# Kernel optimization log

Hardware: AMD Instinct MI355X
Metric: run time of the kernel (lower is better)

Reference implementation:

```python
import jax, jax.numpy as jnp
import numpy as np

B, S, D = 4, 4096, 1024
DC = 1024  # d_chunk (defaults to d_model)
NUM_CLASSES = 4


def setup_inputs() -> dict:
    key = jax.random.key(0)
    ks = jax.random.split(key, 8)
    init = lambda k, shape: (jax.random.normal(k, shape, jnp.float32) * 0.02)
    return {
        "h": jax.random.normal(ks[0], (B, S, D), jnp.float32),
        "pseudo_labels": jax.random.randint(ks[1], (B, S), 0, NUM_CLASSES, jnp.int32),
        "Wl": init(ks[2], (D, NUM_CLASSES)), "bl": jnp.zeros((NUM_CLASSES,), jnp.float32),
        "Wq": init(ks[3], (D, DC)), "bq": jnp.zeros((DC,), jnp.float32),
        "Wk": init(ks[4], (D, DC)), "bk": jnp.zeros((DC,), jnp.float32),
        "Wv": init(ks[5], (D, D)), "bv": jnp.zeros((D,), jnp.float32),
        "Wo": init(ks[6], (D, D)), "bo": jnp.zeros((D,), jnp.float32),
    }


def _chunk_starts(labels):
    """BIOS chunking: label 0=B starts a chunk extended by following 1=I's;
    labels 1 (orphan I), 2=O, 3=S are singleton chunks. Returns bool [B,S]
    marking chunk starts. Parallel replacement for the torch while-loop."""
    def step(ext, lab):  # ext[b]: previous token can be extended by an I
        cont = (lab == 1) & ext          # this token continues prev chunk
        new_ext = (lab == 0) | cont      # B, or a continuing I, is extendable
        return new_ext, ~cont            # non-continuing token starts a chunk
    init = jnp.zeros(labels.shape[0], dtype=bool)
    _, starts_t = jax.lax.scan(step, init, labels.T)  # scan over seq axis
    return starts_t.T  # [B, S]


def reference(h, pseudo_labels, Wl, bl, Wq, bq, Wk, bk, Wv, bv, Wo, bo):
    b, s, d = h.shape
    dc = Wq.shape[1]

    logits = h @ Wl + bl                                  # [B,S,4]
    logp = jax.nn.log_softmax(logits, axis=-1)
    loss = -jnp.mean(jnp.take_along_axis(logp, pseudo_labels[..., None], axis=-1))

    pred = jnp.argmax(logits, axis=-1).astype(jnp.int32)  # [B,S]
    starts = _chunk_starts(pred)
    seg = jnp.cumsum(starts.astype(jnp.int32), axis=1) - 1  # segment id per token

    # Segment-mean pooling, padded to S possible chunks per batch element.
    seg_sum = jax.vmap(lambda x, ids: jax.ops.segment_sum(x, ids, num_segments=s))(h, seg)
    counts = jax.vmap(lambda ids: jax.ops.segment_sum(jnp.ones((s,), h.dtype), ids, num_segments=s))(seg)
    chunk_emb = seg_sum / jnp.maximum(counts, 1.0)[..., None]  # [B,S,D]
    valid = counts > 0                                         # [B,S]

    q = h @ Wq + bq              # [B,S,DC]
    k = chunk_emb @ Wk + bk      # [B,C,DC]
    v = chunk_emb @ Wv + bv      # [B,C,D]
    scale = jnp.asarray(1.0 / np.sqrt(dc), h.dtype)
    scores = jnp.einsum('bsd,bcd->bsc', q, k) * scale
    scores = jnp.where(valid[:, None, :], scores, jnp.asarray(-1e30, h.dtype))
    attn = jax.nn.softmax(scores, axis=-1)
    attended = jnp.einsum('bsc,bcd->bsd', attn, v)
    ch_out = attended @ Wo + bo
    return ch_out, loss
```

## Files before the change

kernel.cpp:

```cpp
#include <hip/hip_runtime.h>

typedef unsigned short u16;
typedef __attribute__((ext_vector_type(8))) short short8;
typedef __attribute__((ext_vector_type(8))) unsigned short ushort8;
typedef __attribute__((ext_vector_type(4))) unsigned short ushort4v;
typedef __attribute__((ext_vector_type(4))) float f32x4;

#define NB 4
#define SS 4096
#define DD 1024
#define CFENCE asm volatile("" ::: "memory")

__device__ __forceinline__ u16 f2bf(float x) {
  unsigned u = __builtin_bit_cast(unsigned, x);
  u = (u + 0x7FFFu + ((u >> 16) & 1u)) >> 16;
  return (u16)u;
}
__device__ __forceinline__ float bf2f(u16 b) {
  unsigned u = ((unsigned)b) << 16;
  return __builtin_bit_cast(float, u);
}
__device__ __forceinline__ void gload16(const void* g, void* l) {
  __builtin_amdgcn_global_load_lds((const __attribute__((address_space(1))) void*)g,
                                   (__attribute__((address_space(3))) void*)l, 16, 0, 0);
}
__device__ __forceinline__ int xcd_swz(int bid, int nwg) {
  const int x = bid & 7, idx = bid >> 3;
  const int q = nwg >> 3, r = nwg & 7;
  return (x < r ? x * (q + 1) : r * (q + 1) + (x - r) * q) + idx;
}

__global__ __launch_bounds__(256) void k_logits(
    const float* __restrict__ h, const int* __restrict__ lab,
    const float* __restrict__ Wl, const float* __restrict__ bl,
    u16* __restrict__ h16, int* __restrict__ pred, float* __restrict__ lossPart)
{
  const int t = threadIdx.x, w = t >> 6, lane = t & 63;
  const int tok = blockIdx.x * 4 + w;
  const float4* h4p = (const float4*)(h + (size_t)tok * DD);
  const float4* wl4 = (const float4*)Wl;
  float p0 = 0.f, p1 = 0.f, p2 = 0.f, p3 = 0.f;
#pragma unroll
  for (int i = 0; i < 4; ++i) {
    const int d = i * 256 + lane * 4;
    float4 hv = h4p[i * 64 + lane];
    ushort4v hb;
    hb[0] = f2bf(hv.x); hb[1] = f2bf(hv.y); hb[2] = f2bf(hv.z); hb[3] = f2bf(hv.w);
    *(ushort4v*)(h16 + (size_t)tok * DD + d) = hb;
    float4 w0 = wl4[d], w1 = wl4[d + 1], w2 = wl4[d + 2], w3 = wl4[d + 3];
    p0 += hv.x * w0.x + hv.y * w1.x + hv.z * w2.x + hv.w * w3.x;
    p1 += hv.x * w0.y + hv.y * w1.y + hv.z * w2.y + hv.w * w3.y;
    p2 += hv.x * w0.z + hv.y * w1.z + hv.z * w2.z + hv.w * w3.z;
    p3 += hv.x * w0.w + hv.y * w1.w + hv.z * w2.w + hv.w * w3.w;
  }
#pragma unroll
  for (int m = 32; m; m >>= 1) {
    p0 += __shfl_xor(p0, m); p1 += __shfl_xor(p1, m);
    p2 += __shfl_xor(p2, m); p3 += __shfl_xor(p3, m);
  }
  __shared__ float ls[4];
  if (lane == 0) {
    float l[4] = {p0 + bl[0], p1 + bl[1], p2 + bl[2], p3 + bl[3]};
    int bi = 0; float bv = l[0];
#pragma unroll
    for (int c = 1; c < 4; ++c) if (l[c] > bv) { bv = l[c]; bi = c; }
    pred[tok] = bi;
    float se = 0.f;
#pragma unroll
    for (int c = 0; c < 4; ++c) se += expf(l[c] - bv);
    float lse = bv + logf(se);
    ls[w] = lse - l[lab[tok]];
  }
  __syncthreads();
  if (t == 0) lossPart[blockIdx.x] = ls[0] + ls[1] + ls[2] + ls[3];
}

__global__ __launch_bounds__(256) void k_wconv(
    const float* __restrict__ W0, const float* __restrict__ W1,
    const float* __restrict__ W2, const float* __restrict__ W3,
    u16* __restrict__ Wt)
{
  const int gid = blockIdx.x * 256 + threadIdx.x;
  const int mat = gid >> 20;
  const int rem = gid & ((1 << 20) - 1);
  const int n = rem >> 10, k = rem & 1023;
  const float* W = (mat == 0) ? W0 : (mat == 1) ? W1 : (mat == 2) ? W2 : W3;
  Wt[((size_t)mat << 20) + (size_t)n * 1024 + k] = f2bf(W[(size_t)k * 1024 + n]);
}

__global__ __launch_bounds__(256) void k_scan(
    const int* __restrict__ pred, int* __restrict__ cstart, int* __restrict__ ccnt)
{
  const int b = blockIdx.x, t = threadIdx.x;
  const int4* p4 = (const int4*)(pred + (size_t)b * SS);
  int labv[16];
#pragma unroll
  for (int i = 0; i < 4; ++i) {
    int4 v = p4[t * 4 + i];
    labv[i * 4 + 0] = v.x; labv[i * 4 + 1] = v.y;
    labv[i * 4 + 2] = v.z; labv[i * 4 + 3] = v.w;
  }
  int A = 0, Bc = 1;
#pragma unroll
  for (int e = 0; e < 16; ++e) {
    int a = (labv[e] == 0), bb = (labv[e] == 1);
    A = a | (bb & A);
    Bc = bb & Bc;
  }
  __shared__ int sA[256], sB[256], sC[256];
  sA[t] = A; sB[t] = Bc;
  __syncthreads();
  for (int off = 1; off < 256; off <<= 1) {
    int pa = 0, pb = 1;
    if (t >= off) { pa = sA[t - off]; pb = sB[t - off]; }
    __syncthreads();
    A = A | (Bc & pa); Bc = Bc & pb;
    sA[t] = A; sB[t] = Bc;
    __syncthreads();
  }
  const int extIn = (t == 0) ? 0 : sA[t - 1];
  int ext = extIn, nst = 0;
#pragma unroll
  for (int e = 0; e < 16; ++e) {
    int cont = (labv[e] == 1) & ext;
    nst += !cont;
    ext = (labv[e] == 0) | cont;
  }
  sC[t] = nst;
  __syncthreads();
  int tot = nst;
  for (int off = 1; off < 256; off <<= 1) {
    int pc = 0;
    if (t >= off) pc = sC[t - off];
    __syncthreads();
    tot += pc;
    sC[t] = tot;
    __syncthreads();
  }
  const int base = tot - nst;
  const int total = sC[255];
  if (t == 0) { ccnt[b] = total; cstart[b * (SS + 1) + total] = SS; }
  ext = extIn; int id = base;
#pragma unroll
  for (int e = 0; e < 16; ++e) {
    int cont = (labv[e] == 1) & ext;
    if (!cont) cstart[b * (SS + 1) + id++] = t * 16 + e;
    ext = (labv[e] == 0) | cont;
  }
}

__global__ __launch_bounds__(256) void k_pool(
    const float* __restrict__ h, const int* __restrict__ cstart,
    const int* __restrict__ ccnt, u16* __restrict__ cemb)
{
  const int t = threadIdx.x, w = t >> 6, lane = t & 63;
  const int gw = blockIdx.x * 4 + w;
  const int b = gw >> 12, c = gw & (SS - 1);
  u16* out = cemb + (size_t)gw * DD + lane * 16;
  if (c >= ccnt[b]) {
    ushort8 z = {0, 0, 0, 0, 0, 0, 0, 0};
    *(ushort8*)out = z; *(ushort8*)(out + 8) = z;
    return;
  }
  const int s0 = cstart[b * (SS + 1) + c], s1 = cstart[b * (SS + 1) + c + 1];
  float acc[16] = {};
  for (int s = s0; s < s1; ++s) {
    const float4* hp = (const float4*)(h + ((size_t)b * SS + s) * DD + lane * 16);
#pragma unroll
    for (int ii = 0; ii < 4; ++ii) {
      float4 v = hp[ii];
      acc[ii * 4 + 0] += v.x; acc[ii * 4 + 1] += v.y;
      acc[ii * 4 + 2] += v.z; acc[ii * 4 + 3] += v.w;
    }
  }
  const float inv = 1.f / (float)(s1 - s0);
  ushort8 o0, o1;
#pragma unroll
  for (int e = 0; e < 8; ++e) { o0[e] = f2bf(acc[e] * inv); o1[e] = f2bf(acc[8 + e] * inv); }
  *(ushort8*)out = o0; *(ushort8*)(out + 8) = o1;
}

template <int OUTF32>
__global__ __launch_bounds__(512, 2) void gemm256(
    const u16* __restrict__ A0p, const u16* __restrict__ A1p,
    const u16* __restrict__ A2p, const u16* __restrict__ A3p,
    const u16* __restrict__ Bt, long strideB,
    void* __restrict__ C0, void* __restrict__ C1,
    void* __restrict__ C2, void* __restrict__ C3,
    const float* __restrict__ bias, float scale, int M, int N, int K)
{
  __shared__ u16 lds[65536];
  u16* ldsA = lds;
  u16* ldsB = lds + 32768;
  const int t = threadIdx.x, lane = t & 63, w = t >> 6;
  const int wr = w >> 2, wc = w & 3;
  const int z = blockIdx.z;
  const u16* A = (z == 0) ? A0p : (z == 1) ? A1p : (z == 2) ? A2p : A3p;
  void* Cp    = (z == 0) ? C0 : (z == 1) ? C1 : (z == 2) ? C2 : C3;
  const u16* B = Bt + (size_t)z * strideB;
  const int bid = blockIdx.y * gridDim.x + blockIdx.x;
  const int swz = xcd_swz(bid, gridDim.x * gridDim.y);
  const int m0 = (swz / gridDim.x) * 256, n0 = (swz % gridDim.x) * 256;

  f32x4 acc[8][4];
#pragma unroll
  for (int i = 0; i < 8; ++i)
#pragma unroll
    for (int j = 0; j < 4; ++j) acc[i][j] = (f32x4){0.f, 0.f, 0.f, 0.f};

  const int trow = t >> 3;
  const u16* Ag = A + (size_t)(m0 + trow) * K + ((t & 7) ^ (trow & 7)) * 8;
  const u16* Bg = B + (size_t)(n0 + trow) * K + ((t & 7) ^ (trow & 7)) * 8;
  u16* dA = ldsA + t * 8;
  u16* dB = ldsB + t * 8;

#define STG_A0(BUF, KT) { gload16(Ag + (size_t)(KT),            dA + (BUF) * 16384 + 0 * 4096); \
                          gload16(Ag + (size_t)128 * K + (KT),  dA + (BUF) * 16384 + 2 * 4096); }
#define STG_A1(BUF, KT) { gload16(Ag + (size_t)64 * K + (KT),   dA + (BUF) * 16384 + 1 * 4096); \
                          gload16(Ag + (size_t)192 * K + (KT),  dA + (BUF) * 16384 + 3 * 4096); }
#define STG_B0(BUF, KT) { gload16(Bg + (size_t)(KT),            dB + (BUF) * 16384 + 0 * 4096); \
                          gload16(Bg + (size_t)64 * K + (KT),   dB + (BUF) * 16384 + 1 * 4096); }
#define STG_B1(BUF, KT) { gload16(Bg + (size_t)128 * K + (KT),  dB + (BUF) * 16384 + 2 * 4096); \
                          gload16(Bg + (size_t)192 * K + (KT),  dB + (BUF) * 16384 + 3 * 4096); }
#define RD_A(DST, BASE, ROFF) \
  { _Pragma("unroll") for (int mi = 0; mi < 4; ++mi) { \
      DST[mi][0] = *(const short8*)((BASE) + (wr * 128 + (ROFF) + mi * 16 + lrow) * 64 + co0); \
      DST[mi][1] = *(const short8*)((BASE) + (wr * 128 + (ROFF) + mi * 16 + lrow) * 64 + co1); } }
#define RD_B(DST, BASE, ROFF) \
  { _Pragma("unroll") for (int ni = 0; ni < 2; ++ni) { \
      DST[ni][0] = *(const short8*)((BASE) + ((ROFF) + wc * 32 + ni * 16 + lrow) * 64 + co0); \
      DST[ni][1] = *(const short8*)((BASE) + ((ROFF) + wc * 32 + ni * 16 + lrow) * 64 + co1); } }
#define MFMA16(MH, AF, BF, NOFF) \
  { _Pragma("unroll") for (int ks = 0; ks < 2; ++ks) \
    _Pragma("unroll") for (int mi = 0; mi < 4; ++mi) \
      _Pragma("unroll") for (int ni = 0; ni < 2; ++ni) \
        acc[(MH) * 4 + mi][(NOFF) + ni] = __builtin_amdgcn_mfma_f32_16x16x32_bf16( \
            AF[mi][ks], BF[ni][ks], acc[(MH) * 4 + mi][(NOFF) + ni], 0, 0, 0); }

  const int lrow = lane & 15, hi = lane >> 4;
  const int co0 = (hi ^ (lrow & 7)) * 8;
  const int co1 = ((4 + hi) ^ (lrow & 7)) * 8;

  const int NT = K >> 6;
  STG_A0(0, 0); STG_B0(0, 0); STG_B1(0, 0); STG_A1(0, 0);
  if (NT > 1) {
    STG_A0(1, 64); STG_B0(1, 64); STG_B1(1, 64); STG_A1(1, 64);
    asm volatile("s_waitcnt vmcnt(8)" ::: "memory");
  } else {
    asm volatile("s_waitcnt vmcnt(0)" ::: "memory");
  }
  __builtin_amdgcn_s_barrier();
  CFENCE;
  short8 afA[4][2], afB[4][2], bA[2][2], bB[2][2];
  RD_A(afA, ldsA, 0);
  RD_B(bA, ldsB, 0);
  CFENCE;

  for (int j = 0; j < NT; ++j) {
    const int cur = j & 1;
    const u16* bufA = ldsA + cur * 16384;
    const u16* bufB = ldsB + cur * 16384;
    const u16* nbufA = ldsA + (cur ^ 1) * 16384;
    const u16* nbufB = ldsB + (cur ^ 1) * 16384;
    const int kt2 = (j + 2) << 6;
    RD_B(bB, bufB, 128);
    CFENCE;
    asm volatile("s_waitcnt lgkmcnt(4)" ::: "memory");
    __builtin_amdgcn_sched_barrier(0);
    __builtin_amdgcn_s_setprio(1);
    MFMA16(0, afA, bA, 0);
    __builtin_amdgcn_s_setprio(0);
    __builtin_amdgcn_sched_barrier(0);
    __builtin_amdgcn_s_barrier();
    CFENCE;
    RD_A(afB, bufA, 64);
    if (j + 2 < NT) { STG_A0(cur, kt2); STG_B0(cur, kt2); }
    CFENCE;
    asm volatile("s_waitcnt lgkmcnt(8)" ::: "memory");
    __builtin_amdgcn_sched_barrier(0);
    __builtin_amdgcn_s_setprio(1);
    MFMA16(0, afA, bB, 2);
    __builtin_amdgcn_s_setprio(0);
    __builtin_amdgcn_sched_barrier(0);
    __builtin_amdgcn_s_barrier();
    CFENCE;
    if (j + 2 < NT) STG_B1(cur, kt2);
    CFENCE;
    asm volatile("s_waitcnt lgkmcnt(0)" ::: "memory");
    __builtin_amdgcn_sched_barrier(0);
    __builtin_amdgcn_s_setprio(1);
    MFMA16(1, afB, bB, 2);
    __builtin_amdgcn_s_setprio(0);
    if (j + 1 < NT) {
      if (j + 2 < NT) asm volatile("s_waitcnt vmcnt(6)" ::: "memory");
      else            asm volatile("s_waitcnt vmcnt(0)" ::: "memory");
    }
    __builtin_amdgcn_sched_barrier(0);
    __builtin_amdgcn_s_barrier();
    CFENCE;
    if (j + 2 < NT) STG_A1(cur, kt2);
    CFENCE;
    __builtin_amdgcn_sched_barrier(0);
    __builtin_amdgcn_s_setprio(1);
    MFMA16(1, afB, bA, 0);
    __builtin_amdgcn_s_setprio(0);
    __builtin_amdgcn_sched_barrier(0);
    if (j + 1 < NT) {
      RD_A(afA, nbufA, 0);
      RD_B(bA, nbufB, 0);
    }
    CFENCE;
    __builtin_amdgcn_s_barrier();
    CFENCE;
  }

  if (OUTF32) {
    const int rowb = m0 + wr * 128 + (lane >> 4) * 4;
#pragma unroll
    for (int n = 0; n < 4; ++n) {
      const int col = n0 + (n >> 1) * 128 + wc * 32 + (n & 1) * 16 + (lane & 15);
      const float bv = bias ? bias[col] : 0.f;
#pragma unroll
      for (int m = 0; m < 8; ++m)
#pragma unroll
        for (int q = 0; q < 4; ++q)
          ((float*)Cp)[(size_t)(rowb + m * 16 + q) * N + col] = acc[m][n][q] * scale + bv;
    }
  } else {
    __syncthreads();
    u16* cls = lds;
    const int rowl = wr * 128 + (lane >> 4) * 4;
#pragma unroll
    for (int n = 0; n < 4; ++n) {
      const int coll = (n >> 1) * 128 + wc * 32 + (n & 1) * 16 + (lane & 15);
      const float bv = bias ? bias[n0 + coll] : 0.f;
#pragma unroll
      for (int m = 0; m < 8; ++m)
#pragma unroll
        for (int q = 0; q < 4; ++q) {
          const int row = rowl + m * 16 + q;
          cls[row * 256 + (coll ^ (((row >> 2) & 3) << 4))] = f2bf(acc[m][n][q] * scale + bv);
        }
    }
    __syncthreads();
    u16* Cu = (u16*)Cp;
#pragma unroll
    for (int ps = 0; ps < 16; ++ps) {
      const int f = ps * 512 + t;
      const int row = f >> 5, col8 = (f & 31);
      const int scol8 = col8 ^ (((row >> 2) & 3) << 1);
      *(ushort8*)(Cu + (size_t)(m0 + row) * N + n0 + col8 * 8) =
          *(const ushort8*)(cls + row * 256 + scol8 * 8);
    }
  }
#undef STG_A0
#undef STG_A1
#undef STG_B0
#undef STG_B1
#undef RD_A
#undef RD_B
#undef MFMA16
}

__global__ __launch_bounds__(256) void k_softmax(
    u16* __restrict__ s0, u16* __restrict__ s1,
    u16* __restrict__ s2, u16* __restrict__ s3, const int* __restrict__ ccnt)
{
  const int t = threadIdx.x, lane = t & 63, w = t >> 6;
  const int row = blockIdx.x, b = blockIdx.y;
  u16* sc = (b == 0) ? s0 : (b == 1) ? s1 : (b == 2) ? s2 : s3;
  const int Cb = ccnt[b];
  u16* p = sc + (size_t)row * SS + t * 16;
  ushort8 v0 = *(ushort8*)p, v1 = *(ushort8*)(p + 8);
  float x[16];
#pragma unroll
  for (int e = 0; e < 8; ++e) { x[e] = bf2f(v0[e]); x[8 + e] = bf2f(v1[e]); }
  const int cb0 = t * 16;
  float m = -1e30f;
#pragma unroll
  for (int e = 0; e < 16; ++e) if (cb0 + e < Cb) m = fmaxf(m, x[e]);
#pragma unroll
  for (int off = 32; off; off >>= 1) m = fmaxf(m, __shfl_xor(m, off));
  __shared__ float red[4], red2[4];
  if (lane == 0) red[w] = m;
  __syncthreads();
  m = fmaxf(fmaxf(red[0], red[1]), fmaxf(red[2], red[3]));
  float ssum = 0.f;
#pragma unroll
  for (int e = 0; e < 16; ++e) {
    float ev = (cb0 + e < Cb) ? __expf(x[e] - m) : 0.f;
    x[e] = ev; ssum += ev;
  }
#pragma unroll
  for (int off = 32; off; off >>= 1) ssum += __shfl_xor(ssum, off);
  if (lane == 0) red2[w] = ssum;
  __syncthreads();
  ssum = red2[0] + red2[1] + red2[2] + red2[3];
  const float inv = 1.f / ssum;
#pragma unroll
  for (int e = 0; e < 8; ++e) { v0[e] = f2bf(x[e] * inv); v1[e] = f2bf(x[8 + e] * inv); }
  *(ushort8*)p = v0; *(ushort8*)(p + 8) = v1;
}

__global__ __launch_bounds__(256) void k_transpose(
    const u16* __restrict__ v, u16* __restrict__ vt)
{
  __shared__ u16 ts[64][80];
  const int t = threadIdx.x;
  const int d0 = blockIdx.x * 64, c0 = blockIdx.y * 64, b = blockIdx.z;
#pragma unroll
  for (int p = 0; p < 2; ++p) {
    const int idx = p * 256 + t, r = idx >> 3, cc = idx & 7;
    ushort8 val = *(const ushort8*)(v + ((size_t)b * SS + c0 + r) * DD + d0 + cc * 8);
    *(ushort8*)&ts[r][cc * 8] = val;
  }
  __syncthreads();
#pragma unroll
  for (int p = 0; p < 2; ++p) {
    const int idx = p * 256 + t, r = idx >> 3, cc = idx & 7;
    ushort8 o;
#pragma unroll
    for (int e = 0; e < 8; ++e) o[e] = ts[cc * 8 + e][r];
    *(ushort8*)(vt + ((size_t)b * DD + d0 + r) * SS + c0 + cc * 8) = o;
  }
}

__global__ __launch_bounds__(256) void k_lossfin(
    const float* __restrict__ part, float* __restrict__ out)
{
  const int t = threadIdx.x, lane = t & 63, w = t >> 6;
  float s = 0.f;
  for (int i = t; i < 4096; i += 256) s += part[i];
#pragma unroll
  for (int off = 32; off; off >>= 1) s += __shfl_xor(s, off);
  __shared__ float r[4];
  if (lane == 0) r[w] = s;
  __syncthreads();
  if (t == 0) out[0] = (r[0] + r[1] + r[2] + r[3]) * (1.f / (NB * SS));
}

extern "C" void kernel_launch(void* const* d_in, const int* in_sizes, int n_in,
                              void* d_out, int out_size, void* d_ws, size_t ws_size,
                              hipStream_t stream) {
  const float* h  = (const float*)d_in[0];
  const int* plab = (const int*)d_in[1];
  const float* Wl = (const float*)d_in[2];
  const float* bl = (const float*)d_in[3];
  const float* Wq = (const float*)d_in[4];
  const float* bq = (const float*)d_in[5];
  const float* Wk = (const float*)d_in[6];
  const float* bk = (const float*)d_in[7];
  const float* Wv = (const float*)d_in[8];
  const float* bv = (const float*)d_in[9];
  const float* Wo = (const float*)d_in[10];
  const float* bo = (const float*)d_in[11];
  float* out = (float*)d_out;

  char* ws = (char*)d_ws;
  const size_t SZ = (size_t)NB * SS * DD * 2;
  const size_t SD = (size_t)SS * DD;
  u16* h16      = (u16*)(ws + 0 * SZ);
  u16* cemb     = (u16*)(ws + 1 * SZ);
  u16* q        = (u16*)(ws + 2 * SZ);
  u16* kk       = (u16*)(ws + 3 * SZ);
  u16* vv       = (u16*)(ws + 4 * SZ);
  u16* vt       = (u16*)(ws + 5 * SZ);
  u16* Wt       = (u16*)(ws + 6 * SZ);
  char* ws2     = ws + 6 * SZ + (size_t)4 * 1024 * 1024 * 2;
  int* pred     = (int*)ws2;
  int* cstart   = (int*)(ws2 + 65536);
  int* ccnt     = (int*)(ws2 + 65536 + 4 * (SS + 1) * 4);
  float* lossPart = (float*)(ws2 + 65536 + 4 * (SS + 1) * 4 + 64);
  u16* s0 = (u16*)d_out;
  u16* s1 = (u16*)d_out + (size_t)SS * SS;
  u16* s2 = h16;
  u16* s3 = cemb;
  u16* att = vv;

  k_logits<<<dim3(NB * SS / 4), 256, 0, stream>>>(h, plab, Wl, bl, h16, pred, lossPart);
  k_wconv<<<dim3(4 * 1024 * 1024 / 256), 256, 0, stream>>>(Wq, Wk, Wv, Wo, Wt);
  k_scan<<<dim3(NB), 256, 0, stream>>>(pred, cstart, ccnt);
  k_pool<<<dim3(NB * SS / 4), 256, 0, stream>>>(h, cstart, ccnt, cemb);

  gemm256<0><<<dim3(DD / 256, NB * SS / 256, 1), 512, 0, stream>>>(
      h16, h16, h16, h16, Wt, 0, q, q, q, q, bq, 1.f, NB * SS, DD, DD);
  gemm256<0><<<dim3(DD / 256, NB * SS / 256, 1), 512, 0, stream>>>(
      cemb, cemb, cemb, cemb, Wt + (1 << 20), 0, kk, kk, kk, kk, bk, 1.f, NB * SS, DD, DD);
  gemm256<0><<<dim3(DD / 256, NB * SS / 256, 1), 512, 0, stream>>>(
      cemb, cemb, cemb, cemb, Wt + 2 * (1 << 20), 0, vv, vv, vv, vv, bv, 1.f, NB * SS, DD, DD);
  k_transpose<<<dim3(DD / 64, SS / 64, NB), 256, 0, stream>>>(vv, vt);

  const float scl = 1.f / 32.f;
  gemm256<0><<<dim3(SS / 256, SS / 256, NB), 512, 0, stream>>>(
      q, q + SD, q + 2 * SD, q + 3 * SD, kk, (long)SD,
      s0, s1, s2, s3, nullptr, scl, SS, SS, DD);
  k_softmax<<<dim3(SS, NB), 256, 0, stream>>>(s0, s1, s2, s3, ccnt);
  gemm256<0><<<dim3(DD / 256, SS / 256, NB), 512, 0, stream>>>(
      s0, s1, s2, s3, vt, (long)SD,
      att, att + SD, att + 2 * SD, att + 3 * SD, nullptr, 1.f, SS, DD, SS);
  gemm256<1><<<dim3(DD / 256, NB * SS / 256, 1), 512, 0, stream>>>(
      att, att, att, att, Wt + 3 * (1 << 20), 0, out, out, out, out, bo, 1.f, NB * SS, DD, DD);
  k_lossfin<<<dim3(1), 256, 0, stream>>>(lossPart, out + (size_t)NB * SS * DD);
}
```

Measured before the change: 614.2 us.

## Restructure GEMM main loop into two half-tile phases with full-width B fragments

Replaces the four-phase ping-pong GEMM schedule, which used separate A/B register fragment sets, with a simpler two-phase loop. Each phase loads one A half-tile and all four B column fragments per warp, then issues 32 MFMAs. The warp's N mapping becomes contiguous 64 columns, and the epilogue drops the LDS swizzle on the bf16 output staging. The aim is fewer barriers and fewer LDS fragment reloads per k-step. The cost is losing the register prefetch of the next tile's fragments, so LDS reads are exposed before the MFMAs, and the unswizzled epilogue may suffer bank conflicts.

```diff
diff --git a/kernel.cpp b/kernel.cpp
--- a/kernel.cpp
+++ b/kernel.cpp
@@ -214,111 +214,79 @@
   u16* dA = ldsA + t * 8;
   u16* dB = ldsB + t * 8;
 
-#define STG_A0(BUF, KT) { gload16(Ag + (size_t)(KT),            dA + (BUF) * 16384 + 0 * 4096); \
-                          gload16(Ag + (size_t)128 * K + (KT),  dA + (BUF) * 16384 + 2 * 4096); }
-#define STG_A1(BUF, KT) { gload16(Ag + (size_t)64 * K + (KT),   dA + (BUF) * 16384 + 1 * 4096); \
-                          gload16(Ag + (size_t)192 * K + (KT),  dA + (BUF) * 16384 + 3 * 4096); }
-#define STG_B0(BUF, KT) { gload16(Bg + (size_t)(KT),            dB + (BUF) * 16384 + 0 * 4096); \
-                          gload16(Bg + (size_t)64 * K + (KT),   dB + (BUF) * 16384 + 1 * 4096); }
-#define STG_B1(BUF, KT) { gload16(Bg + (size_t)128 * K + (KT),  dB + (BUF) * 16384 + 2 * 4096); \
-                          gload16(Bg + (size_t)192 * K + (KT),  dB + (BUF) * 16384 + 3 * 4096); }
-#define RD_A(DST, BASE, ROFF) \
+#define STG_AH0(BUF, KT) { gload16(Ag + (size_t)(KT),            dA + (BUF) * 16384 + 0 * 4096); \
+                           gload16(Ag + (size_t)128 * K + (KT),  dA + (BUF) * 16384 + 2 * 4096); }
+#define STG_AH1(BUF, KT) { gload16(Ag + (size_t)64 * K + (KT),   dA + (BUF) * 16384 + 1 * 4096); \
+                           gload16(Ag + (size_t)192 * K + (KT),  dA + (BUF) * 16384 + 3 * 4096); }
+#define STG_B(BUF, KT)   { gload16(Bg + (size_t)(KT),            dB + (BUF) * 16384 + 0 * 4096); \
+                           gload16(Bg + (size_t)64 * K + (KT),   dB + (BUF) * 16384 + 1 * 4096); \
+                           gload16(Bg + (size_t)128 * K + (KT),  dB + (BUF) * 16384 + 2 * 4096); \
+                           gload16(Bg + (size_t)192 * K + (KT),  dB + (BUF) * 16384 + 3 * 4096); }
+#define RD_A(BASE, ROFF) \
   { _Pragma("unroll") for (int mi = 0; mi < 4; ++mi) { \
-      DST[mi][0] = *(const short8*)((BASE) + (wr * 128 + (ROFF) + mi * 16 + lrow) * 64 + co0); \
-      DST[mi][1] = *(const short8*)((BASE) + (wr * 128 + (ROFF) + mi * 16 + lrow) * 64 + co1); } }
-#define RD_B(DST, BASE, ROFF) \
-  { _Pragma("unroll") for (int ni = 0; ni < 2; ++ni) { \
-      DST[ni][0] = *(const short8*)((BASE) + ((ROFF) + wc * 32 + ni * 16 + lrow) * 64 + co0); \
-      DST[ni][1] = *(const short8*)((BASE) + ((ROFF) + wc * 32 + ni * 16 + lrow) * 64 + co1); } }
-#define MFMA16(MH, AF, BF, NOFF) \
+      af[mi][0] = *(const short8*)((BASE) + (wr * 128 + (ROFF) + mi * 16 + lrow) * 64 + co0); \
+      af[mi][1] = *(const short8*)((BASE) + (wr * 128 + (ROFF) + mi * 16 + lrow) * 64 + co1); } }
+#define RD_B(BASE) \
+  { _Pragma("unroll") for (int ni = 0; ni < 4; ++ni) { \
+      bf[ni][0] = *(const short8*)((BASE) + (wc * 64 + ni * 16 + lrow) * 64 + co0); \
+      bf[ni][1] = *(const short8*)((BASE) + (wc * 64 + ni * 16 + lrow) * 64 + co1); } }
+#define MFMA32(MH) \
   { _Pragma("unroll") for (int ks = 0; ks < 2; ++ks) \
     _Pragma("unroll") for (int mi = 0; mi < 4; ++mi) \
-      _Pragma("unroll") for (int ni = 0; ni < 2; ++ni) \
-        acc[(MH) * 4 + mi][(NOFF) + ni] = __builtin_amdgcn_mfma_f32_16x16x32_bf16( \
-            AF[mi][ks], BF[ni][ks], acc[(MH) * 4 + mi][(NOFF) + ni], 0, 0, 0); }
+      _Pragma("unroll") for (int ni = 0; ni < 4; ++ni) \
+        acc[(MH) * 4 + mi][ni] = __builtin_amdgcn_mfma_f32_16x16x32_bf16( \
+            af[mi][ks], bf[ni][ks], acc[(MH) * 4 + mi][ni], 0, 0, 0); }
 
   const int lrow = lane & 15, hi = lane >> 4;
   const int co0 = (hi ^ (lrow & 7)) * 8;
   const int co1 = ((4 + hi) ^ (lrow & 7)) * 8;
 
   const int NT = K >> 6;
-  STG_A0(0, 0); STG_B0(0, 0); STG_B1(0, 0); STG_A1(0, 0);
+  STG_AH0(0, 0); STG_AH1(0, 0); STG_B(0, 0);
   if (NT > 1) {
-    STG_A0(1, 64); STG_B0(1, 64); STG_B1(1, 64); STG_A1(1, 64);
-    asm volatile("s_waitcnt vmcnt(8)" ::: "memory");
+    STG_AH0(1, 64); STG_B(1, 64);
+    asm volatile("s_waitcnt vmcnt(6)" ::: "memory");
   } else {
     asm volatile("s_waitcnt vmcnt(0)" ::: "memory");
   }
   __builtin_amdgcn_s_barrier();
   CFENCE;
-  short8 afA[4][2], afB[4][2], bA[2][2], bB[2][2];
-  RD_A(afA, ldsA, 0);
-  RD_B(bA, ldsB, 0);
-  CFENCE;
-
+
+  short8 af[4][2], bf[4][2];
   for (int j = 0; j < NT; ++j) {
     const int cur = j & 1;
     const u16* bufA = ldsA + cur * 16384;
     const u16* bufB = ldsB + cur * 16384;
-    const u16* nbufA = ldsA + (cur ^ 1) * 16384;
-    const u16* nbufB = ldsB + (cur ^ 1) * 16384;
-    const int kt2 = (j + 2) << 6;
-    RD_B(bB, bufB, 128);
+    RD_A(bufA, 0);
+    RD_B(bufB);
+    if (j + 1 < NT) STG_AH1(cur ^ 1, (j + 1) << 6);
     CFENCE;
-    asm volatile("s_waitcnt lgkmcnt(4)" ::: "memory");
-    __builtin_amdgcn_sched_barrier(0);
+    __builtin_amdgcn_s_barrier();
     __builtin_amdgcn_s_setprio(1);
-    MFMA16(0, afA, bA, 0);
+    MFMA32(0);
     __builtin_amdgcn_s_setprio(0);
     __builtin_amdgcn_sched_barrier(0);
     __builtin_amdgcn_s_barrier();
     CFENCE;
-    RD_A(afB, bufA, 64);
-    if (j + 2 < NT) { STG_A0(cur, kt2); STG_B0(cur, kt2); }
+    RD_A(bufA, 64);
+    if (j + 2 < NT) { STG_AH0(cur, (j + 2) << 6); STG_B(cur, (j + 2) << 6); }
     CFENCE;
-    asm volatile("s_waitcnt lgkmcnt(8)" ::: "memory");
-    __builtin_amdgcn_sched_barrier(0);
+    __builtin_amdgcn_s_barrier();
     __builtin_amdgcn_s_setprio(1);
-    MFMA16(0, afA, bB, 2);
+    MFMA32(1);
     __builtin_amdgcn_s_setprio(0);
+    if (j + 2 < NT)       asm volatile("s_waitcnt vmcnt(6)" ::: "memory");
+    else if (j + 2 == NT) asm volatile("s_waitcnt vmcnt(0)" ::: "memory");
     __builtin_amdgcn_sched_barrier(0);
     __builtin_amdgcn_s_barrier();
     CFENCE;
-    if (j + 2 < NT) STG_B1(cur, kt2);
-    CFENCE;
-    asm volatile("s_waitcnt lgkmcnt(0)" ::: "memory");
-    __builtin_amdgcn_sched_barrier(0);
-    __builtin_amdgcn_s_setprio(1);
-    MFMA16(1, afB, bB, 2);
-    __builtin_amdgcn_s_setprio(0);
-    if (j + 1 < NT) {
-      if (j + 2 < NT) asm volatile("s_waitcnt vmcnt(6)" ::: "memory");
-      else            asm volatile("s_waitcnt vmcnt(0)" ::: "memory");
-    }
-    __builtin_amdgcn_sched_barrier(0);
-    __builtin_amdgcn_s_barrier();
-    CFENCE;
-    if (j + 2 < NT) STG_A1(cur, kt2);
-    CFENCE;
-    __builtin_amdgcn_sched_barrier(0);
-    __builtin_amdgcn_s_setprio(1);
-    MFMA16(1, afB, bA, 0);
-    __builtin_amdgcn_s_setprio(0);
-    __builtin_amdgcn_sched_barrier(0);
-    if (j + 1 < NT) {
-      RD_A(afA, nbufA, 0);
-      RD_B(bA, nbufB, 0);
-    }
-    CFENCE;
-    __builtin_amdgcn_s_barrier();
-    CFENCE;
   }
 
   if (OUTF32) {
     const int rowb = m0 + wr * 128 + (lane >> 4) * 4;
 #pragma unroll
     for (int n = 0; n < 4; ++n) {
-      const int col = n0 + (n >> 1) * 128 + wc * 32 + (n & 1) * 16 + (lane & 15);
+      const int col = n0 + wc * 64 + n * 16 + (lane & 15);
       const float bv = bias ? bias[col] : 0.f;
 #pragma unroll
       for (int m = 0; m < 8; ++m)
@@ -332,34 +300,30 @@
     const int rowl = wr * 128 + (lane >> 4) * 4;
 #pragma unroll
     for (int n = 0; n < 4; ++n) {
-      const int coll = (n >> 1) * 128 + wc * 32 + (n & 1) * 16 + (lane & 15);
+      const int coll = wc * 64 + n * 16 + (lane & 15);
       const float bv = bias ? bias[n0 + coll] : 0.f;
 #pragma unroll
       for (int m = 0; m < 8; ++m)
 #pragma unroll
-        for (int q = 0; q < 4; ++q) {
-          const int row = rowl + m * 16 + q;
-          cls[row * 256 + (coll ^ (((row >> 2) & 3) << 4))] = f2bf(acc[m][n][q] * scale + bv);
-        }
+        for (int q = 0; q < 4; ++q)
+          cls[(rowl + m * 16 + q) * 256 + coll] = f2bf(acc[m][n][q] * scale + bv);
     }
     __syncthreads();
     u16* Cu = (u16*)Cp;
 #pragma unroll
     for (int ps = 0; ps < 16; ++ps) {
       const int f = ps * 512 + t;
-      const int row = f >> 5, col8 = (f & 31);
-      const int scol8 = col8 ^ (((row >> 2) & 3) << 1);
-      *(ushort8*)(Cu + (size_t)(m0 + row) * N + n0 + col8 * 8) =
-          *(const ushort8*)(cls + row * 256 + scol8 * 8);
+      const int row = f >> 5, col8 = (f & 31) * 8;
+      *(ushort8*)(Cu + (size_t)(m0 + row) * N + n0 + col8) =
+          *(const ushort8*)(cls + row * 256 + col8);
     }
   }
-#undef STG_A0
-#undef STG_A1
-#undef STG_B0
-#undef STG_B1
+#undef STG_AH0
+#undef STG_AH1
+#undef STG_B
 #undef RD_A
 #undef RD_B
-#undef MFMA16
+#undef MFMA32
 }
 
 __global__ __launch_bounds__(256) void k_softmax(
```

New measurement: 550.9 us. -10.3%, faster.
